# Kernel optimization log

Hardware: AMD Instinct MI355X
Metric: run time of the kernel (lower is better)

Reference implementation:

```python
import jax, jax.numpy as jnp
import numpy as np

DIM = 1024
NHEAD = 16
HEAD_DIM = DIM // NHEAD


def setup_inputs() -> dict:
    key = jax.random.key(0)
    k_x, k_wqkv, k_bqkv, k_wp, k_bp = jax.random.split(key, 5)
    scale = 1.0 / np.sqrt(DIM)
    return {
        "x": jax.random.normal(k_x, (4, 2048, DIM), dtype=jnp.float32),
        "w_qkv": jax.random.uniform(k_wqkv, (DIM, 3 * DIM), minval=-scale, maxval=scale, dtype=jnp.float32),
        "b_qkv": jax.random.uniform(k_bqkv, (3 * DIM,), minval=-scale, maxval=scale, dtype=jnp.float32),
        "w_proj": jax.random.uniform(k_wp, (DIM, DIM), minval=-scale, maxval=scale, dtype=jnp.float32),
        "b_proj": jax.random.uniform(k_bp, (DIM,), minval=-scale, maxval=scale, dtype=jnp.float32),
    }


def reference(x, w_qkv, b_qkv, w_proj, b_proj):
    B, N, D = x.shape
    # qkv projection: [B,N,3D] -> [3,B,H,N,hd]
    qkv = x @ w_qkv + b_qkv
    qkv = qkv.reshape(B, N, 3, NHEAD, HEAD_DIM).transpose(2, 0, 3, 1, 4)
    q, k, v = qkv[0], qkv[1], qkv[2]
    # naive full attention: scores [B,H,N,N]
    attn = jnp.einsum("bhqd,bhkd->bhqk", q, k) / jnp.sqrt(jnp.float32(HEAD_DIM))
    attn = jax.nn.softmax(attn, axis=-1)
    out = jnp.einsum("bhqk,bhkd->bhqd", attn, v)  # [B,H,N,hd]
    out = out.transpose(0, 2, 1, 3).reshape(B, N, D)
    return out @ w_proj + b_proj
```

## Files before the change

### kernel.cpp

```cpp
#include <hip/hip_runtime.h>
#include <math.h>

#define DIM     1024
#define NHEAD   16
#define HD      64
#define BATCH   4
#define SEQ     2048
#define MTOT    (BATCH * SEQ)
#define QKV_N   (3 * DIM)

typedef __attribute__((ext_vector_type(8))) short bf16x8;
typedef __attribute__((ext_vector_type(4))) float f32x4;
typedef unsigned int u32;
typedef unsigned short u16;

__device__ __forceinline__ u16 f2bf(float f) {
    u32 u = __float_as_uint(f);
    return (u16)((u + 0x7fffu + ((u >> 16) & 1u)) >> 16);
}

__device__ __forceinline__ float exp2_fast(float x) {
    float r; asm("v_exp_f32 %0, %1" : "=v"(r) : "v"(x)); return r;
}

__device__ __forceinline__ u32 cvtpk_bf16(float lo, float hi) {
    u32 r; asm("v_cvt_pk_bf16_f32 %0, %1, %2" : "=v"(r) : "v"(lo), "v"(hi));
    return r;
}

__device__ __forceinline__ void gload_lds16(const u16* g, u16* l) {
    __builtin_amdgcn_global_load_lds((const __attribute__((address_space(1))) u32*)g,
                                     (__attribute__((address_space(3))) u32*)l, 16, 0, 0);
}

__global__ __launch_bounds__(256) void cast_x(const float* __restrict__ in,
                                              u16* __restrict__ out) {
    const int i = (blockIdx.x * 256 + threadIdx.x) * 4;
    const float4 v = *(const float4*)&in[i];
    ushort4 o;
    o.x = f2bf(v.x); o.y = f2bf(v.y); o.z = f2bf(v.z); o.w = f2bf(v.w);
    *(ushort4*)&out[i] = o;
}

__global__ __launch_bounds__(256) void cast_transpose(const float* __restrict__ W,
                                                      u16* __restrict__ Wt,
                                                      int K, int N) {
    __shared__ float Ls[64][65];
    const int k0 = blockIdx.x * 64, n0 = blockIdx.y * 64;
    const int t = threadIdx.x;
    const int r = t >> 4, c4 = (t & 15) << 2;
    #pragma unroll
    for (int i = 0; i < 4; ++i) {
        const float4 v = *(const float4*)&W[(size_t)(k0 + r + i * 16) * N + n0 + c4];
        Ls[r + i * 16][c4 + 0] = v.x; Ls[r + i * 16][c4 + 1] = v.y;
        Ls[r + i * 16][c4 + 2] = v.z; Ls[r + i * 16][c4 + 3] = v.w;
    }
    __syncthreads();
    #pragma unroll
    for (int i = 0; i < 4; ++i) {
        const int nr = r + i * 16;
        ushort4 o;
        o.x = f2bf(Ls[c4 + 0][nr]); o.y = f2bf(Ls[c4 + 1][nr]);
        o.z = f2bf(Ls[c4 + 2][nr]); o.w = f2bf(Ls[c4 + 3][nr]);
        *(ushort4*)&Wt[(size_t)(n0 + nr) * K + k0 + c4] = o;
    }
}

#define GEMM_STAGE(buf, kof, Aptr, Bptr)                                       \
    _Pragma("unroll") for (int i = 0; i < 2; ++i) {                            \
        const int row = w * 32 + i * 16 + (lane >> 2);                         \
        const int slot = (lane & 3) ^ ((row >> 1) & 3);                        \
        gload_lds16(&Aptr[(size_t)(m0 + row) * DIM + (kof) + slot * 8],        \
                    &As[buf][(w * 32 + i * 16) * 32]);                         \
        gload_lds16(&Bptr[(size_t)(n0 + row) * DIM + (kof) + slot * 8],        \
                    &Bs[buf][(w * 32 + i * 16) * 32]);                         \
    }

#define GEMM_MAINLOOP(Aptr, Bptr)                                              \
    __shared__ __align__(16) u16 As[2][128 * 32];                              \
    __shared__ __align__(16) u16 Bs[2][128 * 32];                              \
    const int t = threadIdx.x;                                                 \
    const int lane = t & 63, w = t >> 6;                                       \
    const int n0 = blockIdx.x * 128;                                           \
    const int m0 = blockIdx.y * 128;                                           \
    const int wm = (w & 1) * 64, wn = (w >> 1) * 64;                           \
    const int g = lane >> 4, li = lane & 15;                                   \
    f32x4 acc[4][4];                                                           \
    _Pragma("unroll") for (int mt = 0; mt < 4; ++mt)                           \
        _Pragma("unroll") for (int nt = 0; nt < 4; ++nt)                       \
            acc[mt][nt] = (f32x4){0.f, 0.f, 0.f, 0.f};                         \
    GEMM_STAGE(0, 0, Aptr, Bptr)                                               \
    __syncthreads();                                                           \
    int cur = 0;                                                               \
    for (int k0 = 0; k0 < DIM; k0 += 32) {                                     \
        if (k0 + 32 < DIM) { GEMM_STAGE(cur ^ 1, k0 + 32, Aptr, Bptr) }        \
        bf16x8 a[4], b[4];                                                     \
        _Pragma("unroll") for (int mt = 0; mt < 4; ++mt) {                     \
            const int row = wm + mt * 16 + li;                                 \
            const int slot = g ^ ((row >> 1) & 3);                             \
            a[mt] = *(const bf16x8*)&As[cur][row * 32 + slot * 8];             \
        }                                                                      \
        _Pragma("unroll") for (int nt = 0; nt < 4; ++nt) {                     \
            const int row = wn + nt * 16 + li;                                 \
            const int slot = g ^ ((row >> 1) & 3);                             \
            b[nt] = *(const bf16x8*)&Bs[cur][row * 32 + slot * 8];             \
        }                                                                      \
        _Pragma("unroll") for (int mt = 0; mt < 4; ++mt)                       \
            _Pragma("unroll") for (int nt = 0; nt < 4; ++nt)                   \
                acc[mt][nt] = __builtin_amdgcn_mfma_f32_16x16x32_bf16(         \
                    a[mt], b[nt], acc[mt][nt], 0, 0, 0);                       \
        __syncthreads();                                                       \
        cur ^= 1;                                                              \
    }

#define QSCALE 0.18033688011112042f
__global__ __launch_bounds__(256) void gemm_qkv(
    const u16* __restrict__ A, const u16* __restrict__ Bt,
    const float* __restrict__ bias,
    u16* __restrict__ qo, u16* __restrict__ ko, u16* __restrict__ vo)
{
    GEMM_MAINLOOP(A, Bt)
    #pragma unroll
    for (int nt = 0; nt < 4; ++nt) {
        const int n = n0 + wn + nt * 16 + li;
        const int which = n >> 10;
        const int head  = (n >> 6) & 15;
        const int hd    = n & 63;
        u16* dst = (which == 0) ? qo : (which == 1) ? ko : vo;
        const float scale = (which == 0) ? QSCALE : 1.0f;
        const float bv = bias[n];
        #pragma unroll
        for (int mt = 0; mt < 4; ++mt) {
            #pragma unroll
            for (int r = 0; r < 4; ++r) {
                const int m = m0 + wm + mt * 16 + g * 4 + r;
                const int bb = m >> 11, tok = m & 2047;
                dst[((size_t)(bb * NHEAD + head) * SEQ + tok) * HD + hd] =
                    f2bf((acc[mt][nt][r] + bv) * scale);
            }
        }
    }
}

__global__ __launch_bounds__(256) void gemm_proj(
    const u16* __restrict__ A, const u16* __restrict__ Bt,
    const float* __restrict__ bias, float* __restrict__ out)
{
    GEMM_MAINLOOP(A, Bt)
    #pragma unroll
    for (int nt = 0; nt < 4; ++nt) {
        const int n = n0 + wn + nt * 16 + li;
        const float bv = bias[n];
        #pragma unroll
        for (int mt = 0; mt < 4; ++mt) {
            #pragma unroll
            for (int r = 0; r < 4; ++r) {
                const int m = m0 + wm + mt * 16 + g * 4 + r;
                out[(size_t)m * DIM + n] = acc[mt][nt][r] + bv;
            }
        }
    }
}

#define LSTR 72
#define NKT  (SEQ / 64)
__global__ __launch_bounds__(256) void attn_mfma(
    const u16* __restrict__ q, const u16* __restrict__ k,
    const u16* __restrict__ v, u16* __restrict__ ao)
{
    __shared__ __align__(16) u16 Ks[2][64 * LSTR];
    __shared__ __align__(16) u16 Vt[2][64 * LSTR];

    const int t = threadIdx.x;
    const int lane = t & 63, w = t >> 6;
    const int g = lane >> 4, li = lane & 15;
    const int q0 = blockIdx.x * 128;
    const int bh = blockIdx.y;
    const size_t base = (size_t)bh * SEQ * HD;

    bf16x8 qf[2][2];
    #pragma unroll
    for (int h = 0; h < 2; ++h) {
        const size_t qrow = base + (size_t)(q0 + w * 32 + h * 16 + li) * HD;
        qf[h][0] = *(const bf16x8*)&q[qrow + g * 8];
        qf[h][1] = *(const bf16x8*)&q[qrow + 32 + g * 8];
    }

    float lsum[2] = {0.f, 0.f};
    f32x4 oacc[2][4];
    #pragma unroll
    for (int h = 0; h < 2; ++h)
        #pragma unroll
        for (int nt = 0; nt < 4; ++nt) oacc[h][nt] = (f32x4){0.f, 0.f, 0.f, 0.f};

    const int kk = t >> 2, kh = (t & 3) << 4;
    const int kperm = (kk & 32) | (((kk >> 2) & 3) << 3)
                    | (((kk >> 4) & 1) << 2) | (kk & 3);
    const int vkey = (t & 31) << 1, vh0 = (t >> 5) << 3;

    bf16x8 rk0, rk1, rv0, rv1;
    rk0 = *(const bf16x8*)&k[base + (size_t)kperm * HD + kh];
    rk1 = *(const bf16x8*)&k[base + (size_t)kperm * HD + kh + 8];
    rv0 = *(const bf16x8*)&v[base + (size_t)vkey * HD + vh0];
    rv1 = *(const bf16x8*)&v[base + (size_t)(vkey + 1) * HD + vh0];
    {
        u16* Kn = Ks[0]; u16* Vn = Vt[0];
        *(bf16x8*)&Kn[kk * LSTR + kh]     = rk0;
        *(bf16x8*)&Kn[kk * LSTR + kh + 8] = rk1;
        #pragma unroll
        for (int i = 0; i < 8; ++i) {
            const u32 pk = (u32)(u16)rv0[i] | ((u32)(u16)rv1[i] << 16);
            *(u32*)&Vn[(vh0 + i) * LSTR + vkey] = pk;
        }
    }
    __syncthreads();

    int cur = 0;
    for (int kt = 0; kt < NKT; ++kt) {
        const bool more = (kt + 1 < NKT);
        if (more) {
            const size_t kb = base + (size_t)(kt + 1) * 64 * HD;
            rk0 = *(const bf16x8*)&k[kb + (size_t)kperm * HD + kh];
            rk1 = *(const bf16x8*)&k[kb + (size_t)kperm * HD + kh + 8];
            rv0 = *(const bf16x8*)&v[kb + (size_t)vkey * HD + vh0];
            rv1 = *(const bf16x8*)&v[kb + (size_t)(vkey + 1) * HD + vh0];
        }
        const u16* Kc = Ks[cur];
        const u16* Vc = Vt[cur];

        f32x4 s[2][4];
        #pragma unroll
        for (int nt = 0; nt < 4; ++nt) {
            const bf16x8 kf0 = *(const bf16x8*)&Kc[(nt * 16 + li) * LSTR + g * 8];
            const bf16x8 kf1 = *(const bf16x8*)&Kc[(nt * 16 + li) * LSTR + 32 + g * 8];
            #pragma unroll
            for (int h = 0; h < 2; ++h) {
                f32x4 c = (f32x4){0.f, 0.f, 0.f, 0.f};
                c = __builtin_amdgcn_mfma_f32_16x16x32_bf16(kf0, qf[h][0], c, 0, 0, 0);
                c = __builtin_amdgcn_mfma_f32_16x16x32_bf16(kf1, qf[h][1], c, 0, 0, 0);
                s[h][nt] = c;
            }
        }

        bf16x8 pb[2][2];
        #pragma unroll
        for (int h = 0; h < 2; ++h) {
            float rs = 0.f;
            #pragma unroll
            for (int nt = 0; nt < 4; ++nt)
                #pragma unroll
                for (int r = 0; r < 4; ++r) {
                    const float p = exp2_fast(s[h][nt][r]);
                    s[h][nt][r] = p;
                    rs += p;
                }
            lsum[h] += rs;
            #pragma unroll
            for (int ks = 0; ks < 2; ++ks) {
                union { u32 u[4]; bf16x8 v8; } uu;
                uu.u[0] = cvtpk_bf16(s[h][2 * ks][0],     s[h][2 * ks][1]);
                uu.u[1] = cvtpk_bf16(s[h][2 * ks][2],     s[h][2 * ks][3]);
                uu.u[2] = cvtpk_bf16(s[h][2 * ks + 1][0], s[h][2 * ks + 1][1]);
                uu.u[3] = cvtpk_bf16(s[h][2 * ks + 1][2], s[h][2 * ks + 1][3]);
                pb[h][ks] = uu.v8;
            }
        }

        #pragma unroll
        for (int ks = 0; ks < 2; ++ks) {
            #pragma unroll
            for (int nt = 0; nt < 4; ++nt) {
                const bf16x8 vb = *(const bf16x8*)&Vc[(nt * 16 + li) * LSTR + ks * 32 + g * 8];
                #pragma unroll
                for (int h = 0; h < 2; ++h)
                    oacc[h][nt] = __builtin_amdgcn_mfma_f32_16x16x32_bf16(
                        vb, pb[h][ks], oacc[h][nt], 0, 0, 0);
            }
        }

        if (more) {
            u16* Kn = Ks[cur ^ 1]; u16* Vn = Vt[cur ^ 1];
            *(bf16x8*)&Kn[kk * LSTR + kh]     = rk0;
            *(bf16x8*)&Kn[kk * LSTR + kh + 8] = rk1;
            #pragma unroll
            for (int i = 0; i < 8; ++i) {
                const u32 pk = (u32)(u16)rv0[i] | ((u32)(u16)rv1[i] << 16);
                *(u32*)&Vn[(vh0 + i) * LSTR + vkey] = pk;
            }
        }
        __syncthreads();
        cur ^= 1;
    }

    const int bb = bh >> 4, hh = bh & 15;
    #pragma unroll
    for (int h = 0; h < 2; ++h) {
        float lf = lsum[h];
        lf += __shfl_xor(lf, 16);
        lf += __shfl_xor(lf, 32);
        const float inv = 1.0f / lf;
        const int tok = q0 + w * 32 + h * 16 + li;
        u16* dst = &ao[(size_t)(bb * SEQ + tok) * DIM + hh * HD];
        #pragma unroll
        for (int nt = 0; nt < 4; ++nt) {
            const u32 p0 = cvtpk_bf16(oacc[h][nt][0] * inv, oacc[h][nt][1] * inv);
            const u32 p1 = cvtpk_bf16(oacc[h][nt][2] * inv, oacc[h][nt][3] * inv);
            *(u32*)&dst[nt * 16 + g * 4]     = p0;
            *(u32*)&dst[nt * 16 + g * 4 + 2] = p1;
        }
    }
}

extern "C" void kernel_launch(void* const* d_in, const int* in_sizes, int n_in,
                              void* d_out, int out_size, void* d_ws, size_t ws_size,
                              hipStream_t stream)
{
    const float* x      = (const float*)d_in[0];
    const float* w_qkv  = (const float*)d_in[1];
    const float* b_qkv  = (const float*)d_in[2];
    const float* w_proj = (const float*)d_in[3];
    const float* b_proj = (const float*)d_in[4];
    float* out = (float*)d_out;

    u16* xb  = (u16*)d_ws;
    u16* wqt = xb  + (size_t)MTOT * DIM;
    u16* wpt = wqt + (size_t)QKV_N * DIM;
    u16* qb  = wpt + (size_t)DIM * DIM;
    u16* kb  = qb  + (size_t)MTOT * DIM;
    u16* vb  = kb  + (size_t)MTOT * DIM;
    u16* aob = vb  + (size_t)MTOT * DIM;

    cast_x<<<(MTOT * DIM) / 1024, 256, 0, stream>>>(x, xb);
    cast_transpose<<<dim3(DIM / 64, QKV_N / 64), 256, 0, stream>>>(w_qkv, wqt, DIM, QKV_N);
    cast_transpose<<<dim3(DIM / 64, DIM / 64), 256, 0, stream>>>(w_proj, wpt, DIM, DIM);

    gemm_qkv<<<dim3(QKV_N / 128, MTOT / 128), 256, 0, stream>>>(xb, wqt, b_qkv, qb, kb, vb);
    attn_mfma<<<dim3(SEQ / 128, BATCH * NHEAD), 256, 0, stream>>>(qb, kb, vb, aob);
    gemm_proj<<<dim3(DIM / 128, MTOT / 128), 256, 0, stream>>>(aob, wpt, b_proj, out);
}
```

Before: 205.9 us.

## Store V transposed from QKV GEMM and stage K/V via direct global-to-LDS loads

The QKV GEMM epilogue now writes V in a head-dim-major (transposed) layout with packed bf16 pairs. This lets the attention kernel load K and V tiles with direct global-to-LDS copies into XOR-swizzled unpadded shared memory, replacing the register round-trip and the scalar in-kernel V transpose. It also remaps block indices so neighbouring blocks share the same K/V head, which should help L2 reuse. The risks are the uncoalesced strided V stores in the GEMM epilogue and the need for the host-side launch grid and gload_lds16 helper to match the new scheme.

```diff
diff --git a/kernel.cpp b/kernel.cpp
--- a/kernel.cpp
+++ b/kernel.cpp
@@ -126,17 +126,30 @@
         const int which = n >> 10;
         const int head  = (n >> 6) & 15;
         const int hd    = n & 63;
-        u16* dst = (which == 0) ? qo : (which == 1) ? ko : vo;
-        const float scale = (which == 0) ? QSCALE : 1.0f;
         const float bv = bias[n];
-        #pragma unroll
-        for (int mt = 0; mt < 4; ++mt) {
-            #pragma unroll
-            for (int r = 0; r < 4; ++r) {
-                const int m = m0 + wm + mt * 16 + g * 4 + r;
+        if (which == 2) {
+            #pragma unroll
+            for (int mt = 0; mt < 4; ++mt) {
+                const int m = m0 + wm + mt * 16 + g * 4;
                 const int bb = m >> 11, tok = m & 2047;
-                dst[((size_t)(bb * NHEAD + head) * SEQ + tok) * HD + hd] =
-                    f2bf((acc[mt][nt][r] + bv) * scale);
+                const u32 p0 = cvtpk_bf16(acc[mt][nt][0] + bv, acc[mt][nt][1] + bv);
+                const u32 p1 = cvtpk_bf16(acc[mt][nt][2] + bv, acc[mt][nt][3] + bv);
+                u16* d = &vo[((size_t)(bb * NHEAD + head) * HD + hd) * SEQ + tok];
+                *(u32*)&d[0] = p0;
+                *(u32*)&d[2] = p1;
+            }
+        } else {
+            u16* dst = (which == 0) ? qo : ko;
+            const float scale = (which == 0) ? QSCALE : 1.0f;
+            #pragma unroll
+            for (int mt = 0; mt < 4; ++mt) {
+                #pragma unroll
+                for (int r = 0; r < 4; ++r) {
+                    const int m = m0 + wm + mt * 16 + g * 4 + r;
+                    const int bb = m >> 11, tok = m & 2047;
+                    dst[((size_t)(bb * NHEAD + head) * SEQ + tok) * HD + hd] =
+                        f2bf((acc[mt][nt][r] + bv) * scale);
+                }
             }
         }
     }
@@ -162,21 +175,37 @@
     }
 }
 
-#define LSTR 72
 #define NKT  (SEQ / 64)
+#define ATTN_STAGE(buf, ktile)                                                 \
+    _Pragma("unroll") for (int i = 0; i < 2; ++i) {                            \
+        const int rho = w * 16 + i * 8 + srow;                                 \
+        const int key = (rho & 32) | (((rho >> 2) & 3) << 3)                   \
+                      | (((rho >> 4) & 1) << 2) | (rho & 3);                   \
+        const int sl = (sslot ^ (rho & 7)) << 3;                               \
+        gload_lds16(&kg[(size_t)(ktile) * (64 * HD) + (size_t)key * HD + sl],  \
+                    &Ks[buf][(w * 16 + i * 8) * 64]);                          \
+        gload_lds16(&vg[(size_t)rho * SEQ + (ktile) * 64 + sl],                \
+                    &Vs[buf][(w * 16 + i * 8) * 64]);                          \
+    }
+
 __global__ __launch_bounds__(256) void attn_mfma(
     const u16* __restrict__ q, const u16* __restrict__ k,
     const u16* __restrict__ v, u16* __restrict__ ao)
 {
-    __shared__ __align__(16) u16 Ks[2][64 * LSTR];
-    __shared__ __align__(16) u16 Vt[2][64 * LSTR];
+    __shared__ __align__(16) u16 Ks[2][64 * 64];
+    __shared__ __align__(16) u16 Vs[2][64 * 64];
 
     const int t = threadIdx.x;
     const int lane = t & 63, w = t >> 6;
     const int g = lane >> 4, li = lane & 15;
-    const int q0 = blockIdx.x * 128;
-    const int bh = blockIdx.y;
+
+    int flat = blockIdx.y * 16 + blockIdx.x;
+    flat = (flat & 7) * 128 + (flat >> 3);
+    const int q0 = (flat & 15) * 128;
+    const int bh = flat >> 4;
     const size_t base = (size_t)bh * SEQ * HD;
+    const u16* kg = k + base;
+    const u16* vg = v + (size_t)bh * HD * SEQ;
 
     bf16x8 qf[2][2];
     #pragma unroll
@@ -193,46 +222,25 @@
         #pragma unroll
         for (int nt = 0; nt < 4; ++nt) oacc[h][nt] = (f32x4){0.f, 0.f, 0.f, 0.f};
 
-    const int kk = t >> 2, kh = (t & 3) << 4;
-    const int kperm = (kk & 32) | (((kk >> 2) & 3) << 3)
-                    | (((kk >> 4) & 1) << 2) | (kk & 3);
-    const int vkey = (t & 31) << 1, vh0 = (t >> 5) << 3;
-
-    bf16x8 rk0, rk1, rv0, rv1;
-    rk0 = *(const bf16x8*)&k[base + (size_t)kperm * HD + kh];
-    rk1 = *(const bf16x8*)&k[base + (size_t)kperm * HD + kh + 8];
-    rv0 = *(const bf16x8*)&v[base + (size_t)vkey * HD + vh0];
-    rv1 = *(const bf16x8*)&v[base + (size_t)(vkey + 1) * HD + vh0];
-    {
-        u16* Kn = Ks[0]; u16* Vn = Vt[0];
-        *(bf16x8*)&Kn[kk * LSTR + kh]     = rk0;
-        *(bf16x8*)&Kn[kk * LSTR + kh + 8] = rk1;
-        #pragma unroll
-        for (int i = 0; i < 8; ++i) {
-            const u32 pk = (u32)(u16)rv0[i] | ((u32)(u16)rv1[i] << 16);
-            *(u32*)&Vn[(vh0 + i) * LSTR + vkey] = pk;
-        }
-    }
+    const int srow = lane >> 3;
+    const int sslot = lane & 7;
+    const int x8 = li & 7;
+
+    ATTN_STAGE(0, 0)
     __syncthreads();
 
     int cur = 0;
     for (int kt = 0; kt < NKT; ++kt) {
-        const bool more = (kt + 1 < NKT);
-        if (more) {
-            const size_t kb = base + (size_t)(kt + 1) * 64 * HD;
-            rk0 = *(const bf16x8*)&k[kb + (size_t)kperm * HD + kh];
-            rk1 = *(const bf16x8*)&k[kb + (size_t)kperm * HD + kh + 8];
-            rv0 = *(const bf16x8*)&v[kb + (size_t)vkey * HD + vh0];
-            rv1 = *(const bf16x8*)&v[kb + (size_t)(vkey + 1) * HD + vh0];
-        }
+        if (kt + 1 < NKT) { ATTN_STAGE(cur ^ 1, kt + 1) }
         const u16* Kc = Ks[cur];
-        const u16* Vc = Vt[cur];
+        const u16* Vc = Vs[cur];
 
         f32x4 s[2][4];
         #pragma unroll
         for (int nt = 0; nt < 4; ++nt) {
-            const bf16x8 kf0 = *(const bf16x8*)&Kc[(nt * 16 + li) * LSTR + g * 8];
-            const bf16x8 kf1 = *(const bf16x8*)&Kc[(nt * 16 + li) * LSTR + 32 + g * 8];
+            const int rowb = (nt * 16 + li) << 6;
+            const bf16x8 kf0 = *(const bf16x8*)&Kc[rowb + ((g ^ x8) << 3)];
+            const bf16x8 kf1 = *(const bf16x8*)&Kc[rowb + (((g ^ 4) ^ x8) << 3)];
             #pragma unroll
             for (int h = 0; h < 2; ++h) {
                 f32x4 c = (f32x4){0.f, 0.f, 0.f, 0.f};
@@ -270,22 +278,12 @@
         for (int ks = 0; ks < 2; ++ks) {
             #pragma unroll
             for (int nt = 0; nt < 4; ++nt) {
-                const bf16x8 vb = *(const bf16x8*)&Vc[(nt * 16 + li) * LSTR + ks * 32 + g * 8];
+                const bf16x8 vb = *(const bf16x8*)
+                    &Vc[((nt * 16 + li) << 6) + (((g ^ (ks << 2)) ^ x8) << 3)];
                 #pragma unroll
                 for (int h = 0; h < 2; ++h)
                     oacc[h][nt] = __builtin_amdgcn_mfma_f32_16x16x32_bf16(
                         vb, pb[h][ks], oacc[h][nt], 0, 0, 0);
-            }
-        }
-
-        if (more) {
-            u16* Kn = Ks[cur ^ 1]; u16* Vn = Vt[cur ^ 1];
-            *(bf16x8*)&Kn[kk * LSTR + kh]     = rk0;
-            *(bf16x8*)&Kn[kk * LSTR + kh + 8] = rk1;
-            #pragma unroll
-            for (int i = 0; i < 8; ++i) {
-                const u32 pk = (u32)(u16)rv0[i] | ((u32)(u16)rv1[i] << 16);
-                *(u32*)&Vn[(vh0 + i) * LSTR + vkey] = pk;
             }
         }
         __syncthreads();
```

Measured after the change: 210.2 us. 2.1% more time.
